# Kernel optimization log

Measured on AMD Instinct MI355X. Metric: run time of the kernel, lower is better.

The kernel has to match this reference:

```python
import jax, jax.numpy as jnp
import numpy as np

N, F = 8192, 1024


def _lin_params(key, out_f, in_f):
    kw, kb = jax.random.split(key)
    w = jax.random.normal(kw, (out_f, in_f), dtype=jnp.float32) * 0.02
    b = jax.random.normal(kb, (out_f,), dtype=jnp.float32) * 0.02
    return w, b


def setup_inputs() -> dict:
    key = jax.random.key(0)
    ks = jax.random.split(key, 11)
    X = jax.random.normal(ks[0], (N, F), dtype=jnp.float32)
    A = jax.random.uniform(ks[1], (N, N), dtype=jnp.float32)
    W1_w, W1_b = _lin_params(ks[2], 512, F)
    t1_w, t1_b = _lin_params(ks[3], 1, 512)
    r1_w, r1_b = _lin_params(ks[4], 1, 512)
    W2_w, W2_b = _lin_params(ks[5], 256, 512)
    t2_w, t2_b = _lin_params(ks[6], 1, 256)
    r2_w, r2_b = _lin_params(ks[7], 1, 256)
    W3_w, W3_b = _lin_params(ks[8], 64, 256)
    t3_w, t3_b = _lin_params(ks[9], 1, 64)
    r3_w, r3_b = _lin_params(ks[10], 1, 64)
    return dict(X=X, A=A,
                W1_w=W1_w, W1_b=W1_b, t1_w=t1_w, t1_b=t1_b, r1_w=r1_w, r1_b=r1_b,
                W2_w=W2_w, W2_b=W2_b, t2_w=t2_w, t2_b=t2_b, r2_w=r2_w, r2_b=r2_b,
                W3_w=W3_w, W3_b=W3_b, t3_w=t3_w, t3_b=t3_b, r3_w=r3_w, r3_b=r3_b)


def _gat_layer(H, A, W_w, W_b, t_w, t_b, r_w, r_b):
    Z = jax.nn.relu(H @ W_w.T + W_b)                     # [N, out]
    t = (Z @ t_w.T + t_b)[:, 0]                          # [N] = vkt(Z)
    r = (Z @ r_w.T + r_b)[:, 0]                          # [N] = vkr(Z)
    # M_s = A * vkt(Z).T  -> M_s[i,j] = A[i,j] * t[j]
    # M_r = (A * vkr(Z).T).T -> M_r[i,j] = A[j,i] * r[i]
    M = A * t[None, :] + A.T * r[:, None]
    att = jax.nn.softmax(jax.nn.sigmoid(M), axis=1)      # torch default dim=1 for 2D
    return att @ Z


def reference(X, A,
              W1_w, W1_b, t1_w, t1_b, r1_w, r1_b,
              W2_w, W2_b, t2_w, t2_b, r2_w, r2_b,
              W3_w, W3_b, t3_w, t3_b, r3_w, r3_b):
    H1 = _gat_layer(X, A, W1_w, W1_b, t1_w, t1_b, r1_w, r1_b)
    H2 = _gat_layer(H1, A, W2_w, W2_b, t2_w, t2_b, r2_w, r2_b)
    H3 = _gat_layer(H2, A, W3_w, W3_b, t3_w, t3_b, r3_w, r3_b)
    return H3
```

## Files before the change

kernel.cpp:

```cpp
#include <hip/hip_runtime.h>
#include <math.h>

#define NN 8192

typedef __attribute__((ext_vector_type(8))) short short8;
typedef __attribute__((ext_vector_type(4))) float f32x4;

__device__ __forceinline__ float bf2f(unsigned short u) {
    unsigned int x = ((unsigned int)u) << 16;
    return __builtin_bit_cast(float, x);
}
__device__ __forceinline__ unsigned short f2bf(float f) {
    unsigned int x = __builtin_bit_cast(unsigned int, f);
    x = x + 0x7FFFu + ((x >> 16) & 1u);
    return (unsigned short)(x >> 16);
}
__device__ __forceinline__ float fast_sigexp(float x) {
    float s = __builtin_amdgcn_rcpf(1.0f + __expf(-x));
    return __expf(s);
}
__device__ __forceinline__ void gload16(const void* g, void* l) {
    __builtin_amdgcn_global_load_lds(
        (const __attribute__((address_space(1))) unsigned int*)g,
        (__attribute__((address_space(3))) unsigned int*)l, 16, 0, 0);
}

__global__ __launch_bounds__(256) void cvt_bf16(
    const float* __restrict__ src, unsigned short* __restrict__ dst)
{
    size_t idx = ((size_t)blockIdx.x * 256 + threadIdx.x) * 8;
    float4 a = *(const float4*)(src + idx);
    float4 b = *(const float4*)(src + idx + 4);
    unsigned int w0 = (unsigned int)f2bf(a.x) | ((unsigned int)f2bf(a.y) << 16);
    unsigned int w1 = (unsigned int)f2bf(a.z) | ((unsigned int)f2bf(a.w) << 16);
    unsigned int w2 = (unsigned int)f2bf(b.x) | ((unsigned int)f2bf(b.y) << 16);
    unsigned int w3 = (unsigned int)f2bf(b.z) | ((unsigned int)f2bf(b.w) << 16);
    uint4 o = {w0, w1, w2, w3};
    *(uint4*)(dst + idx) = o;
}

template<typename AT> struct ARow;
template<> struct ARow<unsigned short> {
    struct Raw { uint4 a, b; };
    static __device__ __forceinline__ Raw ld(const unsigned short* p) {
        Raw r; r.a = ((const uint4*)p)[0]; r.b = ((const uint4*)p)[1]; return r;
    }
    static __device__ __forceinline__ void cvt(const Raw& r, float* d) {
        unsigned int wd[8] = {r.a.x, r.a.y, r.a.z, r.a.w, r.b.x, r.b.y, r.b.z, r.b.w};
        #pragma unroll
        for (int k = 0; k < 8; ++k) {
            d[2*k]   = __builtin_bit_cast(float, wd[k] << 16);
            d[2*k+1] = __builtin_bit_cast(float, wd[k] & 0xFFFF0000u);
        }
    }
};
template<> struct ARow<float> {
    struct Raw { float4 v[4]; };
    static __device__ __forceinline__ Raw ld(const float* p) {
        Raw r;
        r.v[0] = ((const float4*)p)[0]; r.v[1] = ((const float4*)p)[1];
        r.v[2] = ((const float4*)p)[2]; r.v[3] = ((const float4*)p)[3];
        return r;
    }
    static __device__ __forceinline__ void cvt(const Raw& r, float* d) {
        #pragma unroll
        for (int q = 0; q < 4; ++q) {
            d[4*q+0] = r.v[q].x; d[4*q+1] = r.v[q].y;
            d[4*q+2] = r.v[q].z; d[4*q+3] = r.v[q].w;
        }
    }
};
template<typename AT> struct StageAc;
template<> struct StageAc<unsigned short> {
    static __device__ __forceinline__ void st(const unsigned short* g, unsigned short* l) {
        uint4 a = ((const uint4*)g)[0];
        uint4 b = ((const uint4*)g)[1];
        unsigned int* d = (unsigned int*)l;
        d[0]=a.x; d[1]=a.y; d[2]=a.z; d[3]=a.w;
        d[4]=b.x; d[5]=b.y; d[6]=b.z; d[7]=b.w;
    }
};
template<> struct StageAc<float> {
    static __device__ __forceinline__ void st(const float* g, unsigned short* l) {
        typename ARow<float>::Raw r = ARow<float>::ld(g);
        float v[16];
        ARow<float>::cvt(r, v);
        unsigned int* d = (unsigned int*)l;
        #pragma unroll
        for (int k = 0; k < 8; ++k)
            d[k] = (unsigned int)f2bf(v[2*k]) | ((unsigned int)f2bf(v[2*k+1]) << 16);
    }
};

__global__ __launch_bounds__(256) void proj_mfma(
    const unsigned short* __restrict__ Hbf,
    const unsigned short* __restrict__ Wbf,
    const float* __restrict__ bias,
    unsigned short* __restrict__ Zt,
    int K, int O)
{
    constexpr int MT = 4, NT = 2;
    __shared__ unsigned short smem[8704];
    unsigned short* As = smem;
    unsigned short* Bs = smem + 4096;
    const int tid = threadIdx.x;
    const int w = tid >> 6;
    const int lane = tid & 63;
    const int quad = lane >> 4;
    const int m16 = lane & 15;
    const int i0 = blockIdx.y * 128;
    const int o0 = blockIdx.x * 64;
    const int wm = w & 1;
    const int wn = w >> 1;

    const char* gpa[2]; void* lpa[2];
    #pragma unroll
    for (int n = 0; n < 2; ++n) {
        int o16 = n * 256 + w * 64 + lane;
        int row = o16 >> 2, ch = o16 & 3;
        int sc = ch ^ ((row >> 1) & 3);
        gpa[n] = (const char*)(Hbf + (size_t)(i0 + row) * K) + sc * 16;
        lpa[n] = (char*)As + n * 4096 + w * 1024 + lane * 16;
    }
    const char* gpb; void* lpb;
    {
        int o16 = w * 64 + lane;
        int row = o16 >> 2, ch = o16 & 3;
        int sc = ch ^ ((row >> 1) & 3);
        gpb = (const char*)(Wbf + (size_t)(o0 + row) * K) + sc * 16;
        lpb = (char*)Bs + w * 1024 + lane * 16;
    }
    int aoff[MT], boff[NT];
    #pragma unroll
    for (int mt = 0; mt < MT; ++mt) {
        int row = wm * 64 + mt * 16 + m16;
        int sc = quad ^ ((row >> 1) & 3);
        aoff[mt] = row * 32 + sc * 8;
    }
    #pragma unroll
    for (int nt = 0; nt < NT; ++nt) {
        int row = wn * 32 + nt * 16 + m16;
        int sc = quad ^ ((row >> 1) & 3);
        boff[nt] = row * 32 + sc * 8;
    }
    f32x4 acc[MT][NT];
    #pragma unroll
    for (int mt = 0; mt < MT; ++mt)
        #pragma unroll
        for (int nt = 0; nt < NT; ++nt)
            acc[mt][nt] = (f32x4){0.f, 0.f, 0.f, 0.f};

    for (int k0 = 0; k0 < K; k0 += 32) {
        gload16(gpa[0], lpa[0]); gpa[0] += 64;
        gload16(gpa[1], lpa[1]); gpa[1] += 64;
        gload16(gpb, lpb); gpb += 64;
        __syncthreads();
        short8 af[MT], bf_[NT];
        #pragma unroll
        for (int mt = 0; mt < MT; ++mt) af[mt] = *(const short8*)(As + aoff[mt]);
        #pragma unroll
        for (int nt = 0; nt < NT; ++nt) bf_[nt] = *(const short8*)(Bs + boff[nt]);
        #pragma unroll
        for (int mt = 0; mt < MT; ++mt)
            #pragma unroll
            for (int nt = 0; nt < NT; ++nt)
                acc[mt][nt] = __builtin_amdgcn_mfma_f32_16x16x32_bf16(
                    af[mt], bf_[nt], acc[mt][nt], 0, 0, 0);
        __syncthreads();
    }
    #pragma unroll
    for (int nt = 0; nt < NT; ++nt) {
        int ol = wn * 32 + nt * 16 + m16;
        float bv = bias[o0 + ol];
        #pragma unroll
        for (int mt = 0; mt < MT; ++mt)
            #pragma unroll
            for (int rg = 0; rg < 4; ++rg) {
                int il = wm * 64 + mt * 16 + quad * 4 + rg;
                smem[ol * 136 + il] = f2bf(fmaxf(acc[mt][nt][rg] + bv, 0.f));
            }
    }
    __syncthreads();
    #pragma unroll
    for (int c = 0; c < 4; ++c) {
        int cc = c * 256 + tid;
        int ol = cc >> 4;
        int ic = (cc & 15) << 3;
        *(uint4*)(Zt + (size_t)(o0 + ol) * NN + i0 + ic) = *(const uint4*)&smem[ol * 136 + ic];
    }
}

__global__ __launch_bounds__(256) void tr_zt(
    const unsigned short* __restrict__ Zt,
    const float* __restrict__ tw, const float* __restrict__ tb,
    const float* __restrict__ rw, const float* __restrict__ rb,
    float* __restrict__ t, float* __restrict__ r)
{
    const int i  = blockIdx.x * 256 + threadIdx.x;
    const int c0 = blockIdx.y * 64;
    float at = 0.f, ar = 0.f;
    for (int c = c0; c < c0 + 64; ++c) {
        float z = bf2f(Zt[(size_t)c * NN + i]);
        at = fmaf(z, tw[c], at);
        ar = fmaf(z, rw[c], ar);
    }
    if (blockIdx.y == 0) { at += tb[0]; ar += rb[0]; }
    atomicAdd(t + i, at);
    atomicAdd(r + i, ar);
}

template<int BN, typename AT>
__global__ __launch_bounds__(256) void attn_fused(
    const AT* __restrict__ A,
    const unsigned short* __restrict__ Zt,
    const float* __restrict__ t, const float* __restrict__ r,
    float* __restrict__ Hacc, float* __restrict__ denom,
    int O, int kcount)
{
    constexpr int BM = 128, BK = 32;
    constexpr int MT = 4;
    constexpr int NT = BN / 32;
    constexpr int NB = (BN * BK * 2) / 4096;
    constexpr int BNK = BN * BK;
    __shared__ unsigned short As[BM * BK];
    __shared__ unsigned short Bs[2][BNK];
    __shared__ unsigned short Ac[BK * 130];
    const int tid  = threadIdx.x;
    const int w    = tid >> 6;
    const int lane = tid & 63;
    const int quad = lane >> 4;
    const int m16  = lane & 15;
    const int i0 = blockIdx.y * BM;
    const int c0 = blockIdx.x * BN;
    const int wm = w & 1;
    const int wn = w >> 1;
    const int jbase = blockIdx.z * kcount * BK;

    const int ci = tid >> 1;
    const int jh = tid & 1;
    const float ri = r[i0 + ci];
    const int si = (ci >> 1) & 3;
    unsigned short* asw0 = As + ci * 32 + (((jh * 2)    ) ^ si) * 8;
    unsigned short* asw1 = As + ci * 32 + (((jh * 2) + 1) ^ si) * 8;
    const int sj = tid >> 3;
    const int sm = tid & 7;
    unsigned short* acw = Ac + sj * 130 + sm * 16;
    const AT* astage = A + (size_t)(jbase + sj) * NN + i0 + sm * 16;

    const char* gpb[NB]; unsigned int lob[NB];
    #pragma unroll
    for (int n = 0; n < NB; ++n) {
        int o16 = n * 256 + w * 64 + lane;
        int row = o16 >> 2, ch = o16 & 3;
        int sc = ch ^ ((row >> 1) & 3);
        gpb[n] = (const char*)Zt + ((size_t)(c0 + row) * NN + jbase) * 2 + sc * 16;
        lob[n] = n * 4096 + w * 1024 + lane * 16;
    }
    int aoff[MT], boff[NT];
    #pragma unroll
    for (int mt = 0; mt < MT; ++mt) {
        int row = wm * 64 + mt * 16 + m16;
        int sc = quad ^ ((row >> 1) & 3);
        aoff[mt] = row * 32 + sc * 8;
    }
    #pragma unroll
    for (int nt = 0; nt < NT; ++nt) {
        int row = wn * (BN / 2) + nt * 16 + m16;
        int sc = quad ^ ((row >> 1) & 3);
        boff[nt] = row * 32 + sc * 8;
    }

    f32x4 acc[MT][NT];
    #pragma unroll
    for (int mt = 0; mt < MT; ++mt)
        #pragma unroll
        for (int nt = 0; nt < NT; ++nt)
            acc[mt][nt] = (f32x4){0.f, 0.f, 0.f, 0.f};

    const AT* arow = A + (size_t)(i0 + ci) * NN + jbase + jh * 16;
    const float* tptr = t + jbase + jh * 16;

    #pragma unroll
    for (int n = 0; n < NB; ++n)
        gload16(gpb[n], (char*)Bs[0] + lob[n]);
    StageAc<AT>::st(astage, acw);
    typename ARow<AT>::Raw avr = ARow<AT>::ld(arow);
    float4 tvr0 = ((const float4*)tptr)[0];
    float4 tvr1 = ((const float4*)tptr)[1];
    float4 tvr2 = ((const float4*)tptr)[2];
    float4 tvr3 = ((const float4*)tptr)[3];
    __syncthreads();

    float rsum = 0.f;
    for (int kk = 0; kk < kcount; ++kk) {
        const int b = kk & 1;
        float av[16], tvv[16];
        ARow<AT>::cvt(avr, av);
        tvv[0]=tvr0.x; tvv[1]=tvr0.y; tvv[2]=tvr0.z; tvv[3]=tvr0.w;
        tvv[4]=tvr1.x; tvv[5]=tvr1.y; tvv[6]=tvr1.z; tvv[7]=tvr1.w;
        tvv[8]=tvr2.x; tvv[9]=tvr2.y; tvv[10]=tvr2.z; tvv[11]=tvr2.w;
        tvv[12]=tvr3.x; tvv[13]=tvr3.y; tvv[14]=tvr3.z; tvv[15]=tvr3.w;
        unsigned int wd[8];
        #pragma unroll
        for (int e = 0; e < 16; ++e) {
            float aji = bf2f(Ac[(jh * 16 + e) * 130 + ci]);
            float x = fmaf(av[e], tvv[e], aji * ri);
            float p = fast_sigexp(x);
            rsum += p;
            if (e & 1) wd[e >> 1] |= ((unsigned int)f2bf(p)) << 16;
            else       wd[e >> 1]  = (unsigned int)f2bf(p);
        }
        {
            uint4 s0 = {wd[0], wd[1], wd[2], wd[3]};
            uint4 s1 = {wd[4], wd[5], wd[6], wd[7]};
            *(uint4*)asw0 = s0;
            *(uint4*)asw1 = s1;
        }
        __syncthreads();
        {
            const unsigned short* bsb = Bs[b];
            short8 af[MT], bf_[NT];
            #pragma unroll
            for (int mt = 0; mt < MT; ++mt) af[mt] = *(const short8*)(As + aoff[mt]);
            #pragma unroll
            for (int nt = 0; nt < NT; ++nt) bf_[nt] = *(const short8*)(bsb + boff[nt]);
            #pragma unroll
            for (int mt = 0; mt < MT; ++mt)
                #pragma unroll
                for (int nt = 0; nt < NT; ++nt)
                    acc[mt][nt] = __builtin_amdgcn_mfma_f32_16x16x32_bf16(
                        af[mt], bf_[nt], acc[mt][nt], 0, 0, 0);
        }
        if (kk + 1 < kcount) {
            #pragma unroll
            for (int n = 0; n < NB; ++n)
                gload16(gpb[n] + (size_t)(kk + 1) * 64, (char*)Bs[b ^ 1] + lob[n]);
            StageAc<AT>::st(astage + (size_t)(kk + 1) * BK * NN, acw);
            avr = ARow<AT>::ld(arow + (size_t)(kk + 1) * BK);
            const float* tp = tptr + (kk + 1) * BK;
            tvr0 = ((const float4*)tp)[0];
            tvr1 = ((const float4*)tp)[1];
            tvr2 = ((const float4*)tp)[2];
            tvr3 = ((const float4*)tp)[3];
        }
        __syncthreads();
    }

    rsum += __shfl_xor(rsum, 1);
    if (jh == 0 && blockIdx.x == 0)
        atomicAdd(denom + i0 + ci, rsum);

    const int colb = c0 + wn * (BN / 2) + m16;
    #pragma unroll
    for (int mt = 0; mt < MT; ++mt) {
        int rowb = i0 + wm * 64 + mt * 16 + quad * 4;
        #pragma unroll
        for (int rg = 0; rg < 4; ++rg) {
            float* orow = Hacc + (size_t)(rowb + rg) * O + colb;
            #pragma unroll
            for (int nt = 0; nt < NT; ++nt)
                atomicAdd(orow + nt * 16, acc[mt][nt][rg]);
        }
    }
}

__global__ __launch_bounds__(256) void norm_cvt(
    const float* __restrict__ Hacc, const float* __restrict__ denom,
    float* __restrict__ outf, unsigned short* __restrict__ outb, int O)
{
    const int gid = blockIdx.x * 256 + threadIdx.x;
    const int n4 = O >> 2;
    const int i = gid / n4;
    const int c = (gid % n4) << 2;
    float inv = __builtin_amdgcn_rcpf(denom[i]);
    float4 v = *(const float4*)(Hacc + (size_t)i * O + c);
    v.x *= inv; v.y *= inv; v.z *= inv; v.w *= inv;
    if (outf) {
        *(float4*)(outf + (size_t)i * O + c) = v;
    } else {
        ushort4 h;
        h.x = f2bf(v.x); h.y = f2bf(v.y); h.z = f2bf(v.z); h.w = f2bf(v.w);
        *(ushort4*)(outb + (size_t)i * O + c) = h;
    }
}

extern "C" void kernel_launch(void* const* d_in, const int* in_sizes, int n_in,
                              void* d_out, int out_size, void* d_ws, size_t ws_size,
                              hipStream_t stream)
{
    (void)in_sizes; (void)n_in; (void)out_size;
    const float* X = (const float*)d_in[0];
    const float* A = (const float*)d_in[1];
    const float* Wws[3] = {(const float*)d_in[2],  (const float*)d_in[8],  (const float*)d_in[14]};
    const float* Wbs[3] = {(const float*)d_in[3],  (const float*)d_in[9],  (const float*)d_in[15]};
    const float* tws[3] = {(const float*)d_in[4],  (const float*)d_in[10], (const float*)d_in[16]};
    const float* tbs[3] = {(const float*)d_in[5],  (const float*)d_in[11], (const float*)d_in[17]};
    const float* rws[3] = {(const float*)d_in[6],  (const float*)d_in[12], (const float*)d_in[18]};
    const float* rbs[3] = {(const float*)d_in[7],  (const float*)d_in[13], (const float*)d_in[19]};
    const int Ks[3] = {1024, 512, 256};
    const int Os[3] = {512, 256, 64};
    const int Zs[3] = {8, 16, 16};
    float* out = (float*)d_out;
    char* ws = (char*)d_ws;
    const size_t MB = (size_t)1 << 20;

    unsigned short* HbfX = (unsigned short*)(ws);
    unsigned short* Hbf2 = (unsigned short*)(ws + 16 * MB);
    unsigned short* Zt   = (unsigned short*)(ws + 24 * MB);
    float*          Hacc = (float*)(ws + 32 * MB);
    unsigned short* Wbf  = (unsigned short*)(ws + 48 * MB);
    float* tv = (float*)(ws + 50 * MB);
    float* rv = tv + NN;
    float* dv = rv + NN;
    unsigned short* Abf = (unsigned short*)(ws + 51 * MB);
    const bool useAbf = (ws_size >= 180 * MB);

    unsigned short* WbfL[3] = {Wbf, Wbf + 512 * 1024, Wbf + 512 * 1024 + 256 * 512};

    cvt_bf16<<<(NN * 1024) / 2048, 256, 0, stream>>>(X, HbfX);
    for (int L = 0; L < 3; ++L)
        cvt_bf16<<<(Os[L] * Ks[L]) / 2048, 256, 0, stream>>>(Wws[L], WbfL[L]);
    if (useAbf)
        cvt_bf16<<<(int)(((size_t)NN * NN) / 2048), 256, 0, stream>>>(A, Abf);

    const unsigned short* Hbf_in = HbfX;
    for (int L = 0; L < 3; ++L) {
        int K = Ks[L], O = Os[L];
        int zs = Zs[L];
        int kcount = NN / (zs * 32);
        proj_mfma<<<dim3(O / 64, NN / 128), 256, 0, stream>>>(
            Hbf_in, WbfL[L], Wbs[L], Zt, K, O);
        hipMemsetAsync(tv, 0, 96 * 1024, stream);
        tr_zt<<<dim3(NN / 256, O / 64), 256, 0, stream>>>(
            Zt, tws[L], tbs[L], rws[L], rbs[L], tv, rv);
        hipMemsetAsync(Hacc, 0, (size_t)NN * O * sizeof(float), stream);
        int gx = (O >= 256) ? O / 256 : 1;
        dim3 grid(gx, NN / 128, zs);
        if (useAbf) {
            if (O >= 256)
                attn_fused<256, unsigned short><<<grid, 256, 0, stream>>>(
                    Abf, Zt, tv, rv, Hacc, dv, O, kcount);
            else
                attn_fused<64, unsigned short><<<grid, 256, 0, stream>>>(
                    Abf, Zt, tv, rv, Hacc, dv, O, kcount);
        } else {
            if (O >= 256)
                attn_fused<256, float><<<grid, 256, 0, stream>>>(
                    A, Zt, tv, rv, Hacc, dv, O, kcount);
            else
                attn_fused<64, float><<<grid, 256, 0, stream>>>(
                    A, Zt, tv, rv, Hacc, dv, O, kcount);
        }
        float* outf = (L == 2) ? out : nullptr;
        unsigned short* outb = (L == 2) ? nullptr : Hbf2;
        norm_cvt<<<(NN / 256) * (O / 4), 256, 0, stream>>>(Hacc, dv, outf, outb, O);
        Hbf_in = Hbf2;
    }
}
```

Before: 956.4 us.

## Double-buffer projection and attention staging, async-load transposed A tile, use packed bf16 cvt

New measurement: 920.3 us. 1.04x faster.

```diff
diff --git a/kernel.cpp b/kernel.cpp
--- a/kernel.cpp
+++ b/kernel.cpp
@@ -10,10 +10,10 @@
     unsigned int x = ((unsigned int)u) << 16;
     return __builtin_bit_cast(float, x);
 }
-__device__ __forceinline__ unsigned short f2bf(float f) {
-    unsigned int x = __builtin_bit_cast(unsigned int, f);
-    x = x + 0x7FFFu + ((x >> 16) & 1u);
-    return (unsigned short)(x >> 16);
+__device__ __forceinline__ unsigned int cvt_pk_bf16(float lo, float hi) {
+    unsigned int r;
+    asm("v_cvt_pk_bf16_f32 %0, %1, %2" : "=v"(r) : "v"(lo), "v"(hi));
+    return r;
 }
 __device__ __forceinline__ float fast_sigexp(float x) {
     float s = __builtin_amdgcn_rcpf(1.0f + __expf(-x));
@@ -31,11 +31,8 @@
     size_t idx = ((size_t)blockIdx.x * 256 + threadIdx.x) * 8;
     float4 a = *(const float4*)(src + idx);
     float4 b = *(const float4*)(src + idx + 4);
-    unsigned int w0 = (unsigned int)f2bf(a.x) | ((unsigned int)f2bf(a.y) << 16);
-    unsigned int w1 = (unsigned int)f2bf(a.z) | ((unsigned int)f2bf(a.w) << 16);
-    unsigned int w2 = (unsigned int)f2bf(b.x) | ((unsigned int)f2bf(b.y) << 16);
-    unsigned int w3 = (unsigned int)f2bf(b.z) | ((unsigned int)f2bf(b.w) << 16);
-    uint4 o = {w0, w1, w2, w3};
+    uint4 o = { cvt_pk_bf16(a.x, a.y), cvt_pk_bf16(a.z, a.w),
+                cvt_pk_bf16(b.x, b.y), cvt_pk_bf16(b.z, b.w) };
     *(uint4*)(dst + idx) = o;
 }
 
@@ -70,25 +67,17 @@
         }
     }
 };
-template<typename AT> struct StageAc;
-template<> struct StageAc<unsigned short> {
-    static __device__ __forceinline__ void st(const unsigned short* g, unsigned short* l) {
-        uint4 a = ((const uint4*)g)[0];
-        uint4 b = ((const uint4*)g)[1];
-        unsigned int* d = (unsigned int*)l;
-        d[0]=a.x; d[1]=a.y; d[2]=a.z; d[3]=a.w;
-        d[4]=b.x; d[5]=b.y; d[6]=b.z; d[7]=b.w;
-    }
-};
-template<> struct StageAc<float> {
-    static __device__ __forceinline__ void st(const float* g, unsigned short* l) {
-        typename ARow<float>::Raw r = ARow<float>::ld(g);
+struct AcStageF32 {
+    static __device__ __forceinline__ void st(const ARow<float>::Raw& rw, unsigned short* dst) {
         float v[16];
-        ARow<float>::cvt(r, v);
-        unsigned int* d = (unsigned int*)l;
-        #pragma unroll
-        for (int k = 0; k < 8; ++k)
-            d[k] = (unsigned int)f2bf(v[2*k]) | ((unsigned int)f2bf(v[2*k+1]) << 16);
+        ARow<float>::cvt(rw, v);
+        unsigned int d[8];
+        #pragma unroll
+        for (int k = 0; k < 8; ++k) d[k] = cvt_pk_bf16(v[2*k], v[2*k+1]);
+        uint4 s0 = {d[0], d[1], d[2], d[3]};
+        uint4 s1 = {d[4], d[5], d[6], d[7]};
+        ((uint4*)dst)[0] = s0;
+        ((uint4*)dst)[1] = s1;
     }
 };
 
@@ -100,9 +89,7 @@
     int K, int O)
 {
     constexpr int MT = 4, NT = 2;
-    __shared__ unsigned short smem[8704];
-    unsigned short* As = smem;
-    unsigned short* Bs = smem + 4096;
+    __shared__ unsigned short smem[12288];
     const int tid = threadIdx.x;
     const int w = tid >> 6;
     const int lane = tid & 63;
@@ -113,22 +100,22 @@
     const int wm = w & 1;
     const int wn = w >> 1;
 
-    const char* gpa[2]; void* lpa[2];
+    const char* gpa[2]; unsigned int loa[2];
     #pragma unroll
     for (int n = 0; n < 2; ++n) {
         int o16 = n * 256 + w * 64 + lane;
         int row = o16 >> 2, ch = o16 & 3;
         int sc = ch ^ ((row >> 1) & 3);
         gpa[n] = (const char*)(Hbf + (size_t)(i0 + row) * K) + sc * 16;
-        lpa[n] = (char*)As + n * 4096 + w * 1024 + lane * 16;
-    }
-    const char* gpb; void* lpb;
+        loa[n] = n * 4096 + w * 1024 + lane * 16;
+    }
+    const char* gpb; unsigned int lob_;
     {
         int o16 = w * 64 + lane;
         int row = o16 >> 2, ch = o16 & 3;
         int sc = ch ^ ((row >> 1) & 3);
         gpb = (const char*)(Wbf + (size_t)(o0 + row) * K) + sc * 16;
-        lpb = (char*)Bs + w * 1024 + lane * 16;
+        lob_ = 8192 + w * 1024 + lane * 16;
     }
     int aoff[MT], boff[NT];
     #pragma unroll
@@ -141,7 +128,7 @@
     for (int nt = 0; nt < NT; ++nt) {
         int row = wn * 32 + nt * 16 + m16;
         int sc = quad ^ ((row >> 1) & 3);
-        boff[nt] = row * 32 + sc * 8;
+        boff[nt] = 4096 + row * 32 + sc * 8;
     }
     f32x4 acc[MT][NT];
     #pragma unroll
@@ -150,16 +137,26 @@
         for (int nt = 0; nt < NT; ++nt)
             acc[mt][nt] = (f32x4){0.f, 0.f, 0.f, 0.f};
 
-    for (int k0 = 0; k0 < K; k0 += 32) {
-        gload16(gpa[0], lpa[0]); gpa[0] += 64;
-        gload16(gpa[1], lpa[1]); gpa[1] += 64;
-        gload16(gpb, lpb); gpb += 64;
-        __syncthreads();
+    gload16(gpa[0], (char*)smem + loa[0]);
+    gload16(gpa[1], (char*)smem + loa[1]);
+    gload16(gpb,    (char*)smem + lob_);
+    __syncthreads();
+
+    const int nk = K >> 5;
+    for (int kk = 0; kk < nk; ++kk) {
+        const int s = kk & 1;
+        if (kk + 1 < nk) {
+            char* dst = (char*)smem + (s ^ 1) * 12288;
+            gload16(gpa[0] + (size_t)(kk + 1) * 64, dst + loa[0]);
+            gload16(gpa[1] + (size_t)(kk + 1) * 64, dst + loa[1]);
+            gload16(gpb    + (size_t)(kk + 1) * 64, dst + lob_);
+        }
+        const unsigned short* buf = smem + s * 6144;
         short8 af[MT], bf_[NT];
         #pragma unroll
-        for (int mt = 0; mt < MT; ++mt) af[mt] = *(const short8*)(As + aoff[mt]);
-        #pragma unroll
-        for (int nt = 0; nt < NT; ++nt) bf_[nt] = *(const short8*)(Bs + boff[nt]);
+        for (int mt = 0; mt < MT; ++mt) af[mt] = *(const short8*)(buf + aoff[mt]);
+        #pragma unroll
+        for (int nt = 0; nt < NT; ++nt) bf_[nt] = *(const short8*)(buf + boff[nt]);
         #pragma unroll
         for (int mt = 0; mt < MT; ++mt)
             #pragma unroll
@@ -173,12 +170,15 @@
         int ol = wn * 32 + nt * 16 + m16;
         float bv = bias[o0 + ol];
         #pragma unroll
-        for (int mt = 0; mt < MT; ++mt)
-            #pragma unroll
-            for (int rg = 0; rg < 4; ++rg) {
-                int il = wm * 64 + mt * 16 + quad * 4 + rg;
-                smem[ol * 136 + il] = f2bf(fmaxf(acc[mt][nt][rg] + bv, 0.f));
-            }
+        for (int mt = 0; mt < MT; ++mt) {
+            int il = wm * 64 + mt * 16 + quad * 4;
+            float f0 = fmaxf(acc[mt][nt][0] + bv, 0.f);
+            float f1 = fmaxf(acc[mt][nt][1] + bv, 0.f);
+            float f2 = fmaxf(acc[mt][nt][2] + bv, 0.f);
+            float f3 = fmaxf(acc[mt][nt][3] + bv, 0.f);
+            uint2 pk = { cvt_pk_bf16(f0, f1), cvt_pk_bf16(f2, f3) };
+            *(uint2*)&smem[ol * 136 + il] = pk;
+        }
     }
     __syncthreads();
     #pragma unroll
@@ -217,6 +217,7 @@
     float* __restrict__ Hacc, float* __restrict__ denom,
     int O, int kcount)
 {
+    constexpr bool BFA = (sizeof(AT) == 2);
     constexpr int BM = 128, BK = 32;
     constexpr int MT = 4;
     constexpr int NT = BN / 32;
@@ -224,7 +225,7 @@
     constexpr int BNK = BN * BK;
     __shared__ unsigned short As[BM * BK];
     __shared__ unsigned short Bs[2][BNK];
-    __shared__ unsigned short Ac[BK * 130];
+    __shared__ unsigned short Ac[2][BK * BM];
     const int tid  = threadIdx.x;
     const int w    = tid >> 6;
     const int lane = tid & 63;
@@ -242,10 +243,7 @@
     const int si = (ci >> 1) & 3;
     unsigned short* asw0 = As + ci * 32 + (((jh * 2)    ) ^ si) * 8;
     unsigned short* asw1 = As + ci * 32 + (((jh * 2) + 1) ^ si) * 8;
-    const int sj = tid >> 3;
-    const int sm = tid & 7;
-    unsigned short* acw = Ac + sj * 130 + sm * 16;
-    const AT* astage = A + (size_t)(jbase + sj) * NN + i0 + sm * 16;
+    const int acrd = jh * 16 * BM + (ci ^ (jh << 5));
 
     const char* gpb[NB]; unsigned int lob[NB];
     #pragma unroll
@@ -256,6 +254,26 @@
         gpb[n] = (const char*)Zt + ((size_t)(c0 + row) * NN + jbase) * 2 + sc * 16;
         lob[n] = n * 4096 + w * 1024 + lane * 16;
     }
+    const char* gpac[2] = {nullptr, nullptr};
+    unsigned int loac[2] = {0, 0};
+    const float* astage = nullptr;
+    int acw_off = 0;
+    if constexpr (BFA) {
+        #pragma unroll
+        for (int n = 0; n < 2; ++n) {
+            int o16 = n * 256 + tid;
+            int row = o16 >> 4;
+            int c16 = (o16 & 15) ^ ((row >> 4) << 2);
+            gpac[n] = (const char*)(A + (size_t)(jbase + row) * NN + i0 + c16 * 8);
+            loac[n] = (unsigned int)(o16 * 16);
+        }
+    } else {
+        const int sj = tid >> 3;
+        const int sm = tid & 7;
+        astage = (const float*)A + (size_t)(jbase + sj) * NN + i0 + sm * 16;
+        acw_off = sj * BM + (((sm * 2) ^ ((sj >> 4) << 2)) * 8);
+    }
+
     int aoff[MT], boff[NT];
     #pragma unroll
     for (int mt = 0; mt < MT; ++mt) {
@@ -282,8 +300,14 @@
 
     #pragma unroll
     for (int n = 0; n < NB; ++n)
-        gload16(gpb[n], (char*)Bs[0] + lob[n]);
-    StageAc<AT>::st(astage, acw);
+        gload16(gpb[n], (char*)(Bs[0]) + lob[n]);
+    if constexpr (BFA) {
+        gload16(gpac[0], (char*)(Ac[0]) + loac[0]);
+        gload16(gpac[1], (char*)(Ac[0]) + loac[1]);
+    } else {
+        ARow<float>::Raw a0 = ARow<float>::ld(astage);
+        AcStageF32::st(a0, &Ac[0][0] + acw_off);
+    }
     typename ARow<AT>::Raw avr = ARow<AT>::ld(arow);
     float4 tvr0 = ((const float4*)tptr)[0];
     float4 tvr1 = ((const float4*)tptr)[1];
@@ -291,24 +315,39 @@
     float4 tvr3 = ((const float4*)tptr)[3];
     __syncthreads();
 
+    ARow<float>::Raw acr;
     float rsum = 0.f;
     for (int kk = 0; kk < kcount; ++kk) {
         const int b = kk & 1;
-        float av[16], tvv[16];
+        if (kk + 1 < kcount) {
+            #pragma unroll
+            for (int n = 0; n < NB; ++n)
+                gload16(gpb[n] + (size_t)(kk + 1) * 64, (char*)(Bs[b ^ 1]) + lob[n]);
+            if constexpr (BFA) {
+                gload16(gpac[0] + (size_t)(kk + 1) * (BK * NN * 2), (char*)(Ac[b ^ 1]) + loac[0]);
+                gload16(gpac[1] + (size_t)(kk + 1) * (BK * NN * 2), (char*)(Ac[b ^ 1]) + loac[1]);
+            } else {
+                acr = ARow<float>::ld(astage + (size_t)(kk + 1) * BK * NN);
+            }
+        }
+        float av[16];
         ARow<AT>::cvt(avr, av);
-        tvv[0]=tvr0.x; tvv[1]=tvr0.y; tvv[2]=tvr0.z; tvv[3]=tvr0.w;
-        tvv[4]=tvr1.x; tvv[5]=tvr1.y; tvv[6]=tvr1.z; tvv[7]=tvr1.w;
-        tvv[8]=tvr2.x; tvv[9]=tvr2.y; tvv[10]=tvr2.z; tvv[11]=tvr2.w;
-        tvv[12]=tvr3.x; tvv[13]=tvr3.y; tvv[14]=tvr3.z; tvv[15]=tvr3.w;
+        float tf[16] = {tvr0.x, tvr0.y, tvr0.z, tvr0.w,
+                        tvr1.x, tvr1.y, tvr1.z, tvr1.w,
+                        tvr2.x, tvr2.y, tvr2.z, tvr2.w,
+                        tvr3.x, tvr3.y, tvr3.z, tvr3.w};
+        const unsigned short* acb = &Ac[b][0] + acrd;
         unsigned int wd[8];
         #pragma unroll
-        for (int e = 0; e < 16; ++e) {
-            float aji = bf2f(Ac[(jh * 16 + e) * 130 + ci]);
-            float x = fmaf(av[e], tvv[e], aji * ri);
-            float p = fast_sigexp(x);
-            rsum += p;
-            if (e & 1) wd[e >> 1] |= ((unsigned int)f2bf(p)) << 16;
-            else       wd[e >> 1]  = (unsigned int)f2bf(p);
+        for (int q = 0; q < 8; ++q) {
+            float j0 = bf2f(acb[(2 * q) * BM]);
+            float j1 = bf2f(acb[(2 * q + 1) * BM]);
+            float x0 = fmaf(av[2 * q],     tf[2 * q],     j0 * ri);
+            float x1 = fmaf(av[2 * q + 1], tf[2 * q + 1], j1 * ri);
+            float p0 = fast_sigexp(x0);
+            float p1 = fast_sigexp(x1);
+            rsum += p0; rsum += p1;
+            wd[q] = cvt_pk_bf16(p0, p1);
         }
         {
             uint4 s0 = {wd[0], wd[1], wd[2], wd[3]};
@@ -317,31 +356,29 @@
             *(uint4*)asw1 = s1;
         }
         __syncthreads();
-        {
-            const unsigned short* bsb = Bs[b];
-            short8 af[MT], bf_[NT];
-            #pragma unroll
-            for (int mt = 0; mt < MT; ++mt) af[mt] = *(const short8*)(As + aoff[mt]);
-            #pragma unroll
-            for (int nt = 0; nt < NT; ++nt) bf_[nt] = *(const short8*)(bsb + boff[nt]);
-            #pragma unroll
-            for (int mt = 0; mt < MT; ++mt)
-                #pragma unroll
-                for (int nt = 0; nt < NT; ++nt)
-                    acc[mt][nt] = __builtin_amdgcn_mfma_f32_16x16x32_bf16(
-                        af[mt], bf_[nt], acc[mt][nt], 0, 0, 0);
-        }
         if (kk + 1 < kcount) {
-            #pragma unroll
-            for (int n = 0; n < NB; ++n)
-                gload16(gpb[n] + (size_t)(kk + 1) * 64, (char*)Bs[b ^ 1] + lob[n]);
-            StageAc<AT>::st(astage + (size_t)(kk + 1) * BK * NN, acw);
             avr = ARow<AT>::ld(arow + (size_t)(kk + 1) * BK);
             const float* tp = tptr + (kk + 1) * BK;
             tvr0 = ((const float4*)tp)[0];
             tvr1 = ((const float4*)tp)[1];
             tvr2 = ((const float4*)tp)[2];
             tvr3 = ((const float4*)tp)[3];
+            if constexpr (!BFA)
+                AcStageF32::st(acr, &Ac[b ^ 1][0] + acw_off);
+        }
+        {
+            const unsigned short* bsb = Bs[b];
+            short8 af[MT], bf_[NT];
+            #pragma unroll
+            for (int mt = 0; mt < MT; ++mt) af[mt] = *(const short8*)(As + aoff[mt]);
+            #pragma unroll
+            for (int nt = 0; nt < NT; ++nt) bf_[nt] = *(const short8*)(bsb + boff[nt]);
+            #pragma unroll
+            for (int mt = 0; mt < MT; ++mt)
+                #pragma unroll
+                for (int nt = 0; nt < NT; ++nt)
+                    acc[mt][nt] = __builtin_amdgcn_mfma_f32_16x16x32_bf16(
+                        af[mt], bf_[nt], acc[mt][nt], 0, 0, 0);
         }
         __syncthreads();
     }
@@ -378,9 +415,8 @@
     if (outf) {
         *(float4*)(outf + (size_t)i * O + c) = v;
     } else {
-        ushort4 h;
-        h.x = f2bf(v.x); h.y = f2bf(v.y); h.z = f2bf(v.z); h.w = f2bf(v.w);
-        *(ushort4*)(outb + (size_t)i * O + c) = h;
+        uint2 o = { cvt_pk_bf16(v.x, v.y), cvt_pk_bf16(v.z, v.w) };
+        *(uint2*)(outb + (size_t)i * O + c) = o;
     }
 }
 
```
